# Kernel optimization log

Hardware: AMD Instinct MI355X
Metric: run time of the kernel (lower is better)

Reference implementation:

```python
import jax, jax.numpy as jnp
import numpy as np

SCALE = 0.08838834764831845  # 1/sqrt(128)
NEG_INF = -1e30


def setup_inputs() -> dict:
    key = jax.random.key(0)
    ks = jax.random.split(key, 6)
    S, Hq, Hkv, D, NB, BS, BMAX, X = 32, 32, 8, 128, 4096, 16, 128, 8
    query = jax.random.normal(ks[0], (S, Hq, D), jnp.float32)
    key_cache = jax.random.normal(ks[1], (NB, Hkv, D // X, BS, X), jnp.float32)
    value_cache = jax.random.normal(ks[2], (NB, Hkv, D, BS), jnp.float32)
    block_tables = jax.random.randint(ks[3], (S, BMAX), 0, NB, dtype=jnp.int32)
    seq_lens = jax.random.randint(ks[4], (S,), 1, BMAX * BS + 1, dtype=jnp.int32)
    alibi_slopes = jax.random.uniform(ks[5], (Hq,), jnp.float32)
    query_start_len = jnp.arange(S + 1, dtype=jnp.int32)  # every seq is a 1-token decode
    return dict(query_ptr=query, key_cache_ptr=key_cache, value_cache_ptr=value_cache,
                block_tables_ptr=block_tables, seq_lens_ptr=seq_lens,
                alibi_slopes_ptr=alibi_slopes, query_start_len_ptr=query_start_len)


def reference(query_ptr, key_cache_ptr, value_cache_ptr, block_tables_ptr,
              seq_lens_ptr, alibi_slopes_ptr, query_start_len_ptr):
    S, Bmax = block_tables_ptr.shape
    NB, Hkv, D0, BS, X = key_cache_ptr.shape
    D = D0 * X
    Hq = query_ptr.shape[1]
    G = Hq // Hkv  # queries per kv head
    Kmax = Bmax * BS

    # de-interleave vLLM K layout [NB,Hkv,D//x,BS,x] -> [NB,Hkv,BS,D]; K[d] = cache[.., d//x, tok, d%x]
    K = key_cache_ptr.transpose(0, 1, 3, 2, 4).reshape(NB, Hkv, BS, D).astype(jnp.float32)
    V = value_cache_ptr.transpose(0, 1, 3, 2).astype(jnp.float32)  # [NB,Hkv,BS,D]

    qstart = query_start_len_ptr[:-1]
    qlen = query_start_len_ptr[1:] - qstart

    q = query_ptr[qstart].astype(jnp.float32).reshape(S, Hkv, G, D)  # one decode token per seq

    # block-table-driven KV gather: [S,Bmax,Hkv,BS,D] -> [S,Hkv,Kmax,D]
    Kg = K[block_tables_ptr].transpose(0, 2, 1, 3, 4).reshape(S, Hkv, Kmax, D)
    Vg = V[block_tables_ptr].transpose(0, 2, 1, 3, 4).reshape(S, Hkv, Kmax, D)

    scores = SCALE * jnp.einsum('shgd,shkd->shgk', q, Kg)  # [S,Hkv,G,Kmax]

    pos = jnp.arange(Kmax, dtype=jnp.float32)
    ctx = (seq_lens_ptr.astype(jnp.float32) - 1.0)[:, None, None, None]
    slopes = alibi_slopes_ptr.reshape(Hkv, G)  # head idx = kv_head*G + q
    bias = slopes[None, :, :, None] * (pos[None, None, None, :] - ctx)
    valid = (jnp.arange(Kmax)[None, :] < seq_lens_ptr[:, None])[:, None, None, :]
    scores = jnp.where(valid, scores + bias, NEG_INF)

    m = jnp.max(scores, axis=-1, keepdims=True)
    p = jnp.exp(scores - m) * valid  # online-softmax numerator
    l = jnp.sum(p, axis=-1, keepdims=True)
    acc = jnp.einsum('shgk,shkd->shgd', p, Vg)
    out = acc / (l + 1e-10)  # matches acc/(L + 1e-10) in source

    decode = (qlen == 1).astype(query_ptr.dtype)  # seqs with query_len>1 are skipped (zeros)
    out = out.reshape(S, Hq, D).astype(query_ptr.dtype) * decode[:, None, None]
    return jnp.zeros_like(query_ptr).at[qstart].set(out)
```

## Files before the change

kernel.cpp:

```cpp
#include <hip/hip_runtime.h>

#define SCALE_F 0.08838834764831845f
#define NEG_INF -1e30f

constexpr int S    = 32;
constexpr int Hq   = 32;
constexpr int Hkv  = 8;
constexpr int G    = 4;
constexpr int D    = 128;
constexpr int BS   = 16;
constexpr int BMAX = 128;
constexpr int KMAX = BMAX * BS;

template<int PARTS>
__global__ __launch_bounds__(256, 3)
void attn_part_kernel(const float* __restrict__ q_ptr,
                      const float* __restrict__ kc,
                      const float* __restrict__ vc,
                      const int*   __restrict__ bt,
                      const int*   __restrict__ slens,
                      const float* __restrict__ slopes,
                      float* __restrict__ part_acc,
                      float* __restrict__ part_m,
                      float* __restrict__ part_l)
{
    constexpr int CHUNK = KMAX / PARTS;
    constexpr int CPB   = CHUNK / BS;
    constexpr int KT    = (CPB < 8) ? CPB : 8;
    constexpr int RPT   = CPB / 2;
    constexpr int VT    = (RPT < 4) ? RPT : 4;

    __shared__ __align__(16) float sm_s[G * CHUNK];
    __shared__ __align__(16) float sm_acc[G * D];

    const int bid  = blockIdx.x;
    const int part = bid % PARTS;
    const int sh   = bid / PARTS;
    const int h    = sh % Hkv;
    const int s    = sh / Hkv;

    const int seq_len   = slens[s];
    const int num_parts = (seq_len + CHUNK - 1) / CHUNK;
    if (part >= num_parts) return;

    const int tid       = threadIdx.x;
    const int kvb0      = part * CPB;
    const int nb_total  = (seq_len + BS - 1) / BS;
    const int cpb_valid = min(CPB, nb_total - kvb0);
    const int lim       = cpb_valid * BS;

    float slope[G];
    #pragma unroll
    for (int g = 0; g < G; ++g) slope[g] = slopes[h * G + g];
    const float ctx = (float)(seq_len - 1);

    int phys[CPB];
    #pragma unroll
    for (int i = 0; i < CPB; ++i) phys[i] = bt[s * BMAX + kvb0 + i];

    const int o = tid >> 4;
    const int t = tid & 15;

    float4 qa[G], qb[G];
    #pragma unroll
    for (int g = 0; g < G; ++g) {
        const float* qp = q_ptr + ((size_t)(s * Hq + h * G + g) * D + t * 8);
        qa[g] = ((const float4*)qp)[0];
        qb[g] = ((const float4*)qp)[1];
    }

    #pragma unroll 1
    for (int base = 0; base < CPB; base += KT) {
        if (base >= cpb_valid) break;
        float4 kA[KT], kB[KT];
        #pragma unroll
        for (int j = 0; j < KT; ++j) {
            const int i = base + j;
            if (i < cpb_valid) {
                const float* kp = kc + ((((size_t)phys[i] * Hkv + h) * (D / 8) + t) * BS + o) * 8;
                kA[j] = ((const float4*)kp)[0];
                kB[j] = ((const float4*)kp)[1];
            }
        }
        #pragma unroll
        for (int j = 0; j < KT; ++j) {
            const int i = base + j;
            if (i < cpb_valid) {
                float sc[G];
                #pragma unroll
                for (int g = 0; g < G; ++g)
                    sc[g] = qa[g].x * kA[j].x + qa[g].y * kA[j].y + qa[g].z * kA[j].z + qa[g].w * kA[j].w
                          + qb[g].x * kB[j].x + qb[g].y * kB[j].y + qb[g].z * kB[j].z + qb[g].w * kB[j].w;
                #pragma unroll
                for (int g = 0; g < G; ++g) {
                    #pragma unroll
                    for (int msk = 8; msk >= 1; msk >>= 1)
                        sc[g] += __shfl_xor(sc[g], msk, 16);
                }
                const int kpos   = (kvb0 + i) * BS + o;
                const bool valid = kpos < seq_len;
                if (t == 0) {
                    #pragma unroll
                    for (int g = 0; g < G; ++g)
                        sm_s[g * CHUNK + i * BS + o] =
                            valid ? (SCALE_F * sc[g] + slope[g] * ((float)kpos - ctx)) : NEG_INF;
                }
            }
        }
    }

    const int d    = tid & 127;
    const int half = tid >> 7;

    float4 v[VT][4];
    #pragma unroll
    for (int r = 0; r < VT; ++r) {
        const int i = half + 2 * r;
        if (i < cpb_valid) {
            const float4* vp = (const float4*)(vc + (((size_t)phys[i] * Hkv + h) * D + d) * BS);
            v[r][0] = vp[0]; v[r][1] = vp[1]; v[r][2] = vp[2]; v[r][3] = vp[3];
        }
    }

    __syncthreads();

    {
        const int g    = tid >> 6;
        const int lane = tid & 63;
        float m = NEG_INF;
        for (int j = lane; j < lim; j += 64) m = fmaxf(m, sm_s[g * CHUNK + j]);
        #pragma unroll
        for (int msk = 32; msk >= 1; msk >>= 1) m = fmaxf(m, __shfl_xor(m, msk, 64));
        float l = 0.f;
        for (int j = lane; j < lim; j += 64) {
            float p = __expf(sm_s[g * CHUNK + j] - m);
            sm_s[g * CHUNK + j] = p;
            l += p;
        }
        #pragma unroll
        for (int msk = 32; msk >= 1; msk >>= 1) l += __shfl_xor(l, msk, 64);
        if (lane == 0) {
            part_m[(sh * PARTS + part) * G + g] = m;
            part_l[(sh * PARTS + part) * G + g] = l;
        }
    }
    __syncthreads();

    float acc[G] = {0.f, 0.f, 0.f, 0.f};

    #pragma unroll 1
    for (int t0 = 0; t0 < RPT; t0 += VT) {
        #pragma unroll
        for (int r = 0; r < VT; ++r) {
            const int i = half + 2 * (t0 + r);
            if (i < cpb_valid) {
                #pragma unroll
                for (int g = 0; g < G; ++g) {
                    const float4* pp = (const float4*)(sm_s + g * CHUNK + i * BS);
                    float4 p0 = pp[0], p1 = pp[1], p2 = pp[2], p3 = pp[3];
                    acc[g] += p0.x * v[r][0].x + p0.y * v[r][0].y + p0.z * v[r][0].z + p0.w * v[r][0].w;
                    acc[g] += p1.x * v[r][1].x + p1.y * v[r][1].y + p1.z * v[r][1].z + p1.w * v[r][1].w;
                    acc[g] += p2.x * v[r][2].x + p2.y * v[r][2].y + p2.z * v[r][2].z + p2.w * v[r][2].w;
                    acc[g] += p3.x * v[r][3].x + p3.y * v[r][3].y + p3.z * v[r][3].z + p3.w * v[r][3].w;
                }
            }
        }
        if (t0 + VT < RPT) {
            #pragma unroll
            for (int r = 0; r < VT; ++r) {
                const int i = half + 2 * (t0 + VT + r);
                if (i < cpb_valid) {
                    const float4* vp = (const float4*)(vc + (((size_t)phys[i] * Hkv + h) * D + d) * BS);
                    v[r][0] = vp[0]; v[r][1] = vp[1]; v[r][2] = vp[2]; v[r][3] = vp[3];
                }
            }
        }
    }

    if (half == 1) {
        #pragma unroll
        for (int g = 0; g < G; ++g) sm_acc[g * D + d] = acc[g];
    }
    __syncthreads();
    if (half == 0) {
        float* outp = part_acc + (size_t)(sh * PARTS + part) * G * D;
        #pragma unroll
        for (int g = 0; g < G; ++g)
            outp[g * D + d] = acc[g] + sm_acc[g * D + d];
    }
}

__global__ __launch_bounds__(512)
void attn_reduce_kernel(const float* __restrict__ part_acc,
                        const float* __restrict__ part_m,
                        const float* __restrict__ part_l,
                        const int*   __restrict__ slens,
                        float* __restrict__ out,
                        int parts, int chunk)
{
    const int sh  = blockIdx.x;
    const int s   = sh / Hkv;
    const int tid = threadIdx.x;
    const int g   = tid >> 7;
    const int d   = tid & 127;

    const int seq_len = slens[s];
    const int np = min(parts, (seq_len + chunk - 1) / chunk);

    float M = NEG_INF;
    for (int p = 0; p < np; ++p)
        M = fmaxf(M, part_m[(sh * parts + p) * G + g]);
    float L = 0.f, acc = 0.f;
    for (int p = 0; p < np; ++p) {
        const float w = __expf(part_m[(sh * parts + p) * G + g] - M);
        L += w * part_l[(sh * parts + p) * G + g];
        acc += w * part_acc[((size_t)(sh * parts + p) * G + g) * D + d];
    }
    out[(size_t)(sh * G + g) * D + d] = acc / (L + 1e-10f);
}

extern "C" void kernel_launch(void* const* d_in, const int* in_sizes, int n_in,
                              void* d_out, int out_size, void* d_ws, size_t ws_size,
                              hipStream_t stream)
{
    const float* q   = (const float*)d_in[0];
    const float* kc  = (const float*)d_in[1];
    const float* vc  = (const float*)d_in[2];
    const int*   bt  = (const int*)d_in[3];
    const int*   sl  = (const int*)d_in[4];
    const float* slp = (const float*)d_in[5];

    auto ws_need = [](int p) {
        return (size_t)S * Hkv * p * G * (D + 2) * sizeof(float);
    };
    int parts = 16;
    while (parts > 1 && ws_need(parts) > ws_size) parts >>= 1;
    const int chunk = KMAX / parts;

    float* part_acc = (float*)d_ws;
    float* part_m   = part_acc + (size_t)S * Hkv * parts * G * D;
    float* part_l   = part_m   + (size_t)S * Hkv * parts * G;

    const dim3 grid1(S * Hkv * parts);
    switch (parts) {
    case 16: attn_part_kernel<16><<<grid1, 256, 0, stream>>>(q, kc, vc, bt, sl, slp, part_acc, part_m, part_l); break;
    case 8:  attn_part_kernel<8> <<<grid1, 256, 0, stream>>>(q, kc, vc, bt, sl, slp, part_acc, part_m, part_l); break;
    case 4:  attn_part_kernel<4> <<<grid1, 256, 0, stream>>>(q, kc, vc, bt, sl, slp, part_acc, part_m, part_l); break;
    case 2:  attn_part_kernel<2> <<<grid1, 256, 0, stream>>>(q, kc, vc, bt, sl, slp, part_acc, part_m, part_l); break;
    default: attn_part_kernel<1> <<<grid1, 256, 0, stream>>>(q, kc, vc, bt, sl, slp, part_acc, part_m, part_l); break;
    }
    attn_reduce_kernel<<<S * Hkv, 512, 0, stream>>>(
        part_acc, part_m, part_l, sl, (float*)d_out, parts, chunk);
}
```

Before: 473.0 us.

## Map each attention partition to one wavefront with double-buffered V prefetch

Replaces the 256-thread-per-partition split kernel with a wave-level kernel. Each 64-lane wavefront independently handles one (sequence, kv-head, partition) with its own shared-memory score buffer, so the block-wide __syncthreads barriers and the cross-half accumulator reduction go away. K loads are fully unrolled per chunk, and V blocks are double-buffered in registers to overlap the next block's loads with the current block's FMAs. Occupancy is raised to 4 blocks per CU and the minimum partition count becomes 4. The cost is higher register pressure, and every wave computes its full chunk even past seq_len, relying on masking.

Measured after the change: 472.6 us. No clear change (-0.1%).

```diff
diff --git a/kernel.cpp b/kernel.cpp
--- a/kernel.cpp
+++ b/kernel.cpp
@@ -13,8 +13,8 @@
 constexpr int KMAX = BMAX * BS;
 
 template<int PARTS>
-__global__ __launch_bounds__(256, 3)
-void attn_part_kernel(const float* __restrict__ q_ptr,
+__global__ __launch_bounds__(256, 4)
+void attn_wave_kernel(const float* __restrict__ q_ptr,
                       const float* __restrict__ kc,
                       const float* __restrict__ vc,
                       const int*   __restrict__ bt,
@@ -24,42 +24,37 @@
                       float* __restrict__ part_m,
                       float* __restrict__ part_l)
 {
-    constexpr int CHUNK = KMAX / PARTS;
-    constexpr int CPB   = CHUNK / BS;
-    constexpr int KT    = (CPB < 8) ? CPB : 8;
-    constexpr int RPT   = CPB / 2;
-    constexpr int VT    = (RPT < 4) ? RPT : 4;
-
-    __shared__ __align__(16) float sm_s[G * CHUNK];
-    __shared__ __align__(16) float sm_acc[G * D];
-
-    const int bid  = blockIdx.x;
-    const int part = bid % PARTS;
-    const int sh   = bid / PARTS;
-    const int h    = sh % Hkv;
-    const int s    = sh / Hkv;
+    constexpr int CHUNKW = KMAX / PARTS;
+    constexpr int NCH    = CHUNKW / 64;
+    constexpr int CPW    = CHUNKW / BS;
+
+    __shared__ float sm_p[4][G * CHUNKW];
+
+    const int wid  = threadIdx.x >> 6;
+    const int lane = threadIdx.x & 63;
+    const int gw   = blockIdx.x * 4 + wid;
+    const int part = gw % PARTS;
+    const int sh   = gw / PARTS;
+    const int h    = sh & (Hkv - 1);
+    const int s    = sh >> 3;
 
     const int seq_len   = slens[s];
-    const int num_parts = (seq_len + CHUNK - 1) / CHUNK;
+    const int num_parts = (seq_len + CHUNKW - 1) / CHUNKW;
     if (part >= num_parts) return;
 
-    const int tid       = threadIdx.x;
-    const int kvb0      = part * CPB;
-    const int nb_total  = (seq_len + BS - 1) / BS;
-    const int cpb_valid = min(CPB, nb_total - kvb0);
-    const int lim       = cpb_valid * BS;
-
-    float slope[G];
-    #pragma unroll
-    for (int g = 0; g < G; ++g) slope[g] = slopes[h * G + g];
-    const float ctx = (float)(seq_len - 1);
-
-    int phys[CPB];
-    #pragma unroll
-    for (int i = 0; i < CPB; ++i) phys[i] = bt[s * BMAX + kvb0 + i];
-
-    const int o = tid >> 4;
-    const int t = tid & 15;
+    float* smp = sm_p[wid];
+
+    int phys[CPW];
+    #pragma unroll
+    for (int i = 0; i < CPW; ++i) phys[i] = bt[s * BMAX + part * CPW + i];
+
+    const float ctx  = (float)(seq_len - 1);
+    const int   pos0 = part * CHUNKW;
+
+    const int o4 = lane >> 4;
+    const int t  = lane & 15;
+
+    const float wslope = slopes[h * G + (t & 3)];
 
     float4 qa[G], qb[G];
     #pragma unroll
@@ -69,124 +64,125 @@
         qb[g] = ((const float4*)qp)[1];
     }
 
-    #pragma unroll 1
-    for (int base = 0; base < CPB; base += KT) {
-        if (base >= cpb_valid) break;
-        float4 kA[KT], kB[KT];
-        #pragma unroll
-        for (int j = 0; j < KT; ++j) {
-            const int i = base + j;
-            if (i < cpb_valid) {
-                const float* kp = kc + ((((size_t)phys[i] * Hkv + h) * (D / 8) + t) * BS + o) * 8;
-                kA[j] = ((const float4*)kp)[0];
-                kB[j] = ((const float4*)kp)[1];
-            }
-        }
-        #pragma unroll
-        for (int j = 0; j < KT; ++j) {
-            const int i = base + j;
-            if (i < cpb_valid) {
-                float sc[G];
+    #pragma unroll
+    for (int c = 0; c < NCH; ++c) {
+        #pragma unroll
+        for (int jb = 0; jb < 4; ++jb) {
+            const float* kbase = kc + ((((size_t)phys[c * 4 + jb] * Hkv + h) * (D / 8) + t) * BS) * 8;
+            float4 kA[4], kB[4];
+            #pragma unroll
+            for (int j2 = 0; j2 < 4; ++j2) {
+                const float* kp = kbase + (j2 * 4 + o4) * 8;
+                kA[j2] = ((const float4*)kp)[0];
+                kB[j2] = ((const float4*)kp)[1];
+            }
+            #pragma unroll
+            for (int j2 = 0; j2 < 4; ++j2) {
+                float sc0 = qa[0].x*kA[j2].x + qa[0].y*kA[j2].y + qa[0].z*kA[j2].z + qa[0].w*kA[j2].w
+                          + qb[0].x*kB[j2].x + qb[0].y*kB[j2].y + qb[0].z*kB[j2].z + qb[0].w*kB[j2].w;
+                float sc1 = qa[1].x*kA[j2].x + qa[1].y*kA[j2].y + qa[1].z*kA[j2].z + qa[1].w*kA[j2].w
+                          + qb[1].x*kB[j2].x + qb[1].y*kB[j2].y + qb[1].z*kB[j2].z + qb[1].w*kB[j2].w;
+                float sc2 = qa[2].x*kA[j2].x + qa[2].y*kA[j2].y + qa[2].z*kA[j2].z + qa[2].w*kA[j2].w
+                          + qb[2].x*kB[j2].x + qb[2].y*kB[j2].y + qb[2].z*kB[j2].z + qb[2].w*kB[j2].w;
+                float sc3 = qa[3].x*kA[j2].x + qa[3].y*kA[j2].y + qa[3].z*kA[j2].z + qa[3].w*kA[j2].w
+                          + qb[3].x*kB[j2].x + qb[3].y*kB[j2].y + qb[3].z*kB[j2].z + qb[3].w*kB[j2].w;
                 #pragma unroll
-                for (int g = 0; g < G; ++g)
-                    sc[g] = qa[g].x * kA[j].x + qa[g].y * kA[j].y + qa[g].z * kA[j].z + qa[g].w * kA[j].w
-                          + qb[g].x * kB[j].x + qb[g].y * kB[j].y + qb[g].z * kB[j].z + qb[g].w * kB[j].w;
-                #pragma unroll
-                for (int g = 0; g < G; ++g) {
-                    #pragma unroll
-                    for (int msk = 8; msk >= 1; msk >>= 1)
-                        sc[g] += __shfl_xor(sc[g], msk, 16);
+                for (int msk = 8; msk >= 1; msk >>= 1) {
+                    sc0 += __shfl_xor(sc0, msk, 16);
+                    sc1 += __shfl_xor(sc1, msk, 16);
+                    sc2 += __shfl_xor(sc2, msk, 16);
+                    sc3 += __shfl_xor(sc3, msk, 16);
                 }
-                const int kpos   = (kvb0 + i) * BS + o;
-                const bool valid = kpos < seq_len;
-                if (t == 0) {
-                    #pragma unroll
-                    for (int g = 0; g < G; ++g)
-                        sm_s[g * CHUNK + i * BS + o] =
-                            valid ? (SCALE_F * sc[g] + slope[g] * ((float)kpos - ctx)) : NEG_INF;
+                if (t < 4) {
+                    const int pl   = c * 64 + (jb * 4 + j2) * 4 + o4;
+                    const int kpos = pos0 + pl;
+                    const float scv = (t == 0) ? sc0 : (t == 1) ? sc1 : (t == 2) ? sc2 : sc3;
+                    smp[t * CHUNKW + pl] =
+                        (kpos < seq_len) ? (SCALE_F * scv + wslope * ((float)kpos - ctx)) : NEG_INF;
                 }
             }
         }
     }
 
-    const int d    = tid & 127;
-    const int half = tid >> 7;
-
-    float4 v[VT][4];
-    #pragma unroll
-    for (int r = 0; r < VT; ++r) {
-        const int i = half + 2 * r;
-        if (i < cpb_valid) {
-            const float4* vp = (const float4*)(vc + (((size_t)phys[i] * Hkv + h) * D + d) * BS);
-            v[r][0] = vp[0]; v[r][1] = vp[1]; v[r][2] = vp[2]; v[r][3] = vp[3];
-        }
-    }
-
-    __syncthreads();
-
+    const int d0 = lane;
+    float4 vreg[2][2][4];
     {
-        const int g    = tid >> 6;
-        const int lane = tid & 63;
+        const float* vb = vc + ((size_t)phys[0] * Hkv + h) * D * BS;
+        #pragma unroll
+        for (int c = 0; c < 4; ++c) {
+            vreg[0][0][c] = ((const float4*)(vb + (size_t)d0 * BS))[c];
+            vreg[0][1][c] = ((const float4*)(vb + (size_t)(d0 + 64) * BS))[c];
+        }
+    }
+
+    {
+        const int gS = lane >> 4;
+        const int u  = lane & 15;
+        float* rowp = smp + gS * CHUNKW;
+
+        float4 sv[NCH];
         float m = NEG_INF;
-        for (int j = lane; j < lim; j += 64) m = fmaxf(m, sm_s[g * CHUNK + j]);
-        #pragma unroll
-        for (int msk = 32; msk >= 1; msk >>= 1) m = fmaxf(m, __shfl_xor(m, msk, 64));
+        #pragma unroll
+        for (int w = 0; w < NCH; ++w) {
+            sv[w] = ((const float4*)(rowp + u * 4 + w * 64))[0];
+            m = fmaxf(m, fmaxf(fmaxf(sv[w].x, sv[w].y), fmaxf(sv[w].z, sv[w].w)));
+        }
+        #pragma unroll
+        for (int msk = 8; msk >= 1; msk >>= 1) m = fmaxf(m, __shfl_xor(m, msk, 16));
+
         float l = 0.f;
-        for (int j = lane; j < lim; j += 64) {
-            float p = __expf(sm_s[g * CHUNK + j] - m);
-            sm_s[g * CHUNK + j] = p;
-            l += p;
-        }
-        #pragma unroll
-        for (int msk = 32; msk >= 1; msk >>= 1) l += __shfl_xor(l, msk, 64);
-        if (lane == 0) {
-            part_m[(sh * PARTS + part) * G + g] = m;
-            part_l[(sh * PARTS + part) * G + g] = l;
-        }
-    }
-    __syncthreads();
-
-    float acc[G] = {0.f, 0.f, 0.f, 0.f};
-
-    #pragma unroll 1
-    for (int t0 = 0; t0 < RPT; t0 += VT) {
-        #pragma unroll
-        for (int r = 0; r < VT; ++r) {
-            const int i = half + 2 * (t0 + r);
-            if (i < cpb_valid) {
-                #pragma unroll
-                for (int g = 0; g < G; ++g) {
-                    const float4* pp = (const float4*)(sm_s + g * CHUNK + i * BS);
-                    float4 p0 = pp[0], p1 = pp[1], p2 = pp[2], p3 = pp[3];
-                    acc[g] += p0.x * v[r][0].x + p0.y * v[r][0].y + p0.z * v[r][0].z + p0.w * v[r][0].w;
-                    acc[g] += p1.x * v[r][1].x + p1.y * v[r][1].y + p1.z * v[r][1].z + p1.w * v[r][1].w;
-                    acc[g] += p2.x * v[r][2].x + p2.y * v[r][2].y + p2.z * v[r][2].z + p2.w * v[r][2].w;
-                    acc[g] += p3.x * v[r][3].x + p3.y * v[r][3].y + p3.z * v[r][3].z + p3.w * v[r][3].w;
-                }
-            }
-        }
-        if (t0 + VT < RPT) {
-            #pragma unroll
-            for (int r = 0; r < VT; ++r) {
-                const int i = half + 2 * (t0 + VT + r);
-                if (i < cpb_valid) {
-                    const float4* vp = (const float4*)(vc + (((size_t)phys[i] * Hkv + h) * D + d) * BS);
-                    v[r][0] = vp[0]; v[r][1] = vp[1]; v[r][2] = vp[2]; v[r][3] = vp[3];
-                }
-            }
-        }
-    }
-
-    if (half == 1) {
-        #pragma unroll
-        for (int g = 0; g < G; ++g) sm_acc[g * D + d] = acc[g];
-    }
-    __syncthreads();
-    if (half == 0) {
-        float* outp = part_acc + (size_t)(sh * PARTS + part) * G * D;
-        #pragma unroll
-        for (int g = 0; g < G; ++g)
-            outp[g * D + d] = acc[g] + sm_acc[g * D + d];
+        #pragma unroll
+        for (int w = 0; w < NCH; ++w) {
+            float4 pv;
+            pv.x = __expf(sv[w].x - m);
+            pv.y = __expf(sv[w].y - m);
+            pv.z = __expf(sv[w].z - m);
+            pv.w = __expf(sv[w].w - m);
+            l += pv.x + pv.y + pv.z + pv.w;
+            ((float4*)(rowp + u * 4 + w * 64))[0] = pv;
+        }
+        #pragma unroll
+        for (int msk = 8; msk >= 1; msk >>= 1) l += __shfl_xor(l, msk, 16);
+
+        if (u == 0) {
+            part_m[(sh * PARTS + part) * G + gS] = m;
+            part_l[(sh * PARTS + part) * G + gS] = l;
+        }
+    }
+
+    float acc0[G] = {0.f, 0.f, 0.f, 0.f};
+    float acc1[G] = {0.f, 0.f, 0.f, 0.f};
+
+    #pragma unroll
+    for (int i = 0; i < CPW; ++i) {
+        const int cb = i & 1;
+        if (i + 1 < CPW) {
+            const float* vb = vc + ((size_t)phys[i + 1] * Hkv + h) * D * BS;
+            #pragma unroll
+            for (int c = 0; c < 4; ++c) {
+                vreg[cb ^ 1][0][c] = ((const float4*)(vb + (size_t)d0 * BS))[c];
+                vreg[cb ^ 1][1][c] = ((const float4*)(vb + (size_t)(d0 + 64) * BS))[c];
+            }
+        }
+        #pragma unroll
+        for (int g = 0; g < G; ++g) {
+            const float4* pp = (const float4*)(smp + g * CHUNKW + i * BS);
+            #pragma unroll
+            for (int c = 0; c < 4; ++c) {
+                const float4 p4 = pp[c];
+                acc0[g] += p4.x * vreg[cb][0][c].x + p4.y * vreg[cb][0][c].y
+                         + p4.z * vreg[cb][0][c].z + p4.w * vreg[cb][0][c].w;
+                acc1[g] += p4.x * vreg[cb][1][c].x + p4.y * vreg[cb][1][c].y
+                         + p4.z * vreg[cb][1][c].z + p4.w * vreg[cb][1][c].w;
+            }
+        }
+    }
+
+    float* outp = part_acc + (size_t)(sh * PARTS + part) * G * D;
+    #pragma unroll
+    for (int g = 0; g < G; ++g) {
+        outp[g * D + d0]      = acc0[g];
+        outp[g * D + d0 + 64] = acc1[g];
     }
 }
 
@@ -234,20 +230,18 @@
         return (size_t)S * Hkv * p * G * (D + 2) * sizeof(float);
     };
     int parts = 16;
-    while (parts > 1 && ws_need(parts) > ws_size) parts >>= 1;
+    while (parts > 4 && ws_need(parts) > ws_size) parts >>= 1;
     const int chunk = KMAX / parts;
 
     float* part_acc = (float*)d_ws;
     float* part_m   = part_acc + (size_t)S * Hkv * parts * G * D;
     float* part_l   = part_m   + (size_t)S * Hkv * parts * G;
 
-    const dim3 grid1(S * Hkv * parts);
+    const dim3 grid1(S * Hkv * parts / 4);
     switch (parts) {
-    case 16: attn_part_kernel<16><<<grid1, 256, 0, stream>>>(q, kc, vc, bt, sl, slp, part_acc, part_m, part_l); break;
-    case 8:  attn_part_kernel<8> <<<grid1, 256, 0, stream>>>(q, kc, vc, bt, sl, slp, part_acc, part_m, part_l); break;
-    case 4:  attn_part_kernel<4> <<<grid1, 256, 0, stream>>>(q, kc, vc, bt, sl, slp, part_acc, part_m, part_l); break;
-    case 2:  attn_part_kernel<2> <<<grid1, 256, 0, stream>>>(q, kc, vc, bt, sl, slp, part_acc, part_m, part_l); break;
-    default: attn_part_kernel<1> <<<grid1, 256, 0, stream>>>(q, kc, vc, bt, sl, slp, part_acc, part_m, part_l); break;
+    case 16: attn_wave_kernel<16><<<grid1, 256, 0, stream>>>(q, kc, vc, bt, sl, slp, part_acc, part_m, part_l); break;
+    case 8:  attn_wave_kernel<8> <<<grid1, 256, 0, stream>>>(q, kc, vc, bt, sl, slp, part_acc, part_m, part_l); break;
+    default: attn_wave_kernel<4> <<<grid1, 256, 0, stream>>>(q, kc, vc, bt, sl, slp, part_acc, part_m, part_l); break;
     }
     attn_reduce_kernel<<<S * Hkv, 512, 0, stream>>>(
         part_acc, part_m, part_l, sl, (float*)d_out, parts, chunk);
```
